# Kernel optimization log

Measured on AMD Instinct MI355X. Metric: run time of the kernel, lower is better.

Reference implementation:

```python
import jax, jax.numpy as jnp
import numpy as np

S_CENTROIDS = 512
RADIUS = 0.5
NSAMPLE = 32
BN_EPS = 1e-5


def farthest_point_sample(xyz, s):
    # xyz: [B, N, 3] -> idx [B, s], deterministic start at index 0
    B, N, _ = xyz.shape

    def step(carry, _):
        dist, far = carry  # dist [B,N], far [B]
        centroid = jnp.take_along_axis(xyz, far[:, None, None], axis=1)  # [B,1,3]
        d = jnp.sum((xyz - centroid) ** 2, axis=-1)  # [B,N]
        dist = jnp.minimum(dist, d)
        nxt = jnp.argmax(dist, axis=-1).astype(jnp.int32)
        return (dist, nxt), far

    init = (jnp.full((B, N), 1e10, dtype=xyz.dtype), jnp.zeros((B,), jnp.int32))
    _, idx = jax.lax.scan(step, init, None, length=s)
    return idx.T  # [B, s]


def query_ball_point(radius, nsample, xyz, new_xyz):
    # xyz [B,N,3], new_xyz [B,S,3] -> group idx [B,S,nsample]
    B, N, _ = xyz.shape
    sqr = jnp.sum((new_xyz[:, :, None, :] - xyz[:, None, :, :]) ** 2, axis=-1)  # [B,S,N]
    gidx = jnp.where(sqr > radius * radius, N, jnp.arange(N, dtype=jnp.int32)[None, None, :])
    gidx = jnp.sort(gidx, axis=-1)[:, :, :nsample]  # closest-index-first valid ids
    first = gidx[:, :, :1]
    gidx = jnp.where(gidx == N, first, gidx)  # pad misses with first neighbor
    return gidx


def bn_relu(h, gamma, beta):
    # training-mode BatchNorm1d over (batch, length) dims of [BS, C, k]
    m = jnp.mean(h, axis=(0, 2), keepdims=True)
    v = jnp.var(h, axis=(0, 2), keepdims=True)
    hn = (h - m) / jnp.sqrt(v + BN_EPS)
    return jax.nn.relu(hn * gamma[None, :, None] + beta[None, :, None])


def setup_inputs() -> dict:
    key = jax.random.key(0)
    k1, k2, k3, k4 = jax.random.split(key, 4)
    B, N, Din, Dout = 16, 2048, 64, 128  # in_channels=2*Din=128
    x = jax.random.normal(k1, (B, Din, N), dtype=jnp.float32)
    coords = jax.random.uniform(k2, (B, N, 3), dtype=jnp.float32, minval=-1.0, maxval=1.0)
    W1 = jax.random.normal(k3, (Dout, 2 * Din), dtype=jnp.float32) * 0.05  # conv1 1x1 kernel
    W2 = jax.random.normal(k4, (Dout, Dout), dtype=jnp.float32) * 0.05    # conv2 1x1 kernel
    gamma1 = jnp.ones((Dout,), jnp.float32); beta1 = jnp.zeros((Dout,), jnp.float32)
    gamma2 = jnp.ones((Dout,), jnp.float32); beta2 = jnp.zeros((Dout,), jnp.float32)
    return {"x": x, "coords": coords, "W1": W1, "W2": W2,
            "gamma1": gamma1, "beta1": beta1, "gamma2": gamma2, "beta2": beta2}


def reference(x, coords, W1, W2, gamma1, beta1, gamma2, beta2):
    B = x.shape[0]
    feats = jnp.transpose(x, (0, 2, 1))  # [B, N, D]

    fidx = farthest_point_sample(coords, S_CENTROIDS)  # [B, s]
    bidx = jnp.arange(B)[:, None]
    new_xyz = coords[bidx, fidx]        # [B, s, 3]
    new_feat = feats[bidx, fidx]        # [B, s, D]

    gidx = query_ball_point(RADIUS, NSAMPLE, coords, new_xyz)  # [B, s, k]
    grouped = feats[jnp.arange(B)[:, None, None], gidx]        # [B, s, k, D]

    center = new_feat[:, :, None, :]
    agg = jnp.concatenate([grouped - center,
                           jnp.broadcast_to(center, grouped.shape)], axis=-1)  # [B, s, k, 2D]

    b, s, k, d = agg.shape
    h = jnp.transpose(agg, (0, 1, 3, 2)).reshape(b * s, d, k)  # [BS, 2D, k]
    h = bn_relu(jnp.einsum('bck,oc->bok', h, W1), gamma1, beta1)
    h = bn_relu(jnp.einsum('bck,oc->bok', h, W2), gamma2, beta2)
    pooled = jnp.max(h, axis=-1)                  # [BS, out]
    new_feature = jnp.transpose(pooled.reshape(b, s, -1), (0, 2, 1))  # [B, out, s]
    return new_xyz, new_feature
```

## Files before the change

kernel.cpp:

```cpp
#include <hip/hip_runtime.h>
#include <cstdint>

typedef unsigned int uint;
typedef unsigned short ushort_t;
typedef unsigned long long ull;
typedef __attribute__((ext_vector_type(8))) short bf16x8;
typedef __attribute__((ext_vector_type(4))) float f32x4;
typedef __attribute__((ext_vector_type(2))) float f32x2;

#define B_   16
#define N_   2048
#define S_   512
#define G_   8192
#define DIN  64
#define DOUT 128
#define K_   32
#define ATS  136
#define ATS1 72

__device__ __forceinline__ uint bf16b(float f) {
  uint u = __float_as_uint(f);
  return (u + 0x7fffu + ((u >> 16) & 1u)) >> 16;
}
__device__ __forceinline__ float bf2f(uint b) { return __uint_as_float(b << 16); }

template<int CTRL, int RM>
__device__ __forceinline__ float dpp_fmax_step(float x) {
  float y = __uint_as_float((uint)__builtin_amdgcn_update_dpp(
      (int)__float_as_uint(x), (int)__float_as_uint(x), CTRL, RM, 0xf, true));
  return fmaxf(x, y);
}

__global__ __launch_bounds__(256) void fps_kernel(const float* __restrict__ coords,
                                                  int* __restrict__ fidx,
                                                  float* __restrict__ out_xyz) {
  int b = blockIdx.x;
  const float* cb = coords + (size_t)b * (N_ * 3);
  __shared__ float sptx[N_], spty[N_], sptz[N_];
  __shared__ ull   skey[2][4];
  __shared__ int   sfar[S_];
  int tid = threadIdx.x, lane = tid & 63, wid = tid >> 6;
  for (int j = tid; j < N_; j += 256) {
    sptx[j] = cb[3 * j]; spty[j] = cb[3 * j + 1]; sptz[j] = cb[3 * j + 2];
  }
  f32x2 px[4], py[4], pz[4], dist[4];
  int j0 = tid * 8;
#pragma unroll
  for (int p = 0; p < 4; ++p) {
    int j = j0 + 2 * p;
    px[p].x = cb[3 * j];     py[p].x = cb[3 * j + 1]; pz[p].x = cb[3 * j + 2];
    px[p].y = cb[3 * j + 3]; py[p].y = cb[3 * j + 4]; pz[p].y = cb[3 * j + 5];
    dist[p].x = 1e10f; dist[p].y = 1e10f;
  }
  float cx = cb[0], cy = cb[1], cz = cb[2];
  uint far = 0;
  __syncthreads();
  for (int s = 0; s < S_; ++s) {
    if (tid == 0) sfar[s] = (int)far;
    f32x2 c2x = {cx, cx}, c2y = {cy, cy}, c2z = {cz, cz};
    float bestv = -1.f; uint bestloc = 0;
#pragma unroll
    for (int p = 0; p < 4; ++p) {
      f32x2 dx, dy, dz, qx, qy, qz, s1, s2;
      asm("v_pk_add_f32 %0, %1, %2 neg_lo:[0,1] neg_hi:[0,1]" : "=v"(dx) : "v"(px[p]), "v"(c2x));
      asm("v_pk_add_f32 %0, %1, %2 neg_lo:[0,1] neg_hi:[0,1]" : "=v"(dy) : "v"(py[p]), "v"(c2y));
      asm("v_pk_add_f32 %0, %1, %2 neg_lo:[0,1] neg_hi:[0,1]" : "=v"(dz) : "v"(pz[p]), "v"(c2z));
      asm("v_pk_mul_f32 %0, %1, %1" : "=v"(qx) : "v"(dx));
      asm("v_pk_mul_f32 %0, %1, %1" : "=v"(qy) : "v"(dy));
      asm("v_pk_mul_f32 %0, %1, %1" : "=v"(qz) : "v"(dz));
      asm("v_pk_add_f32 %0, %1, %2" : "=v"(s1) : "v"(qx), "v"(qy));
      asm("v_pk_add_f32 %0, %1, %2" : "=v"(s2) : "v"(s1), "v"(qz));
      float n0 = fminf(dist[p].x, s2.x);
      float n1 = fminf(dist[p].y, s2.y);
      dist[p].x = n0; dist[p].y = n1;
      bool g0 = n0 > bestv; bestv = g0 ? n0 : bestv; bestloc = g0 ? (uint)(2 * p) : bestloc;
      bool g1 = n1 > bestv; bestv = g1 ? n1 : bestv; bestloc = g1 ? (uint)(2 * p + 1) : bestloc;
    }
    float m = bestv;
    m = dpp_fmax_step<0x111, 0xf>(m);
    m = dpp_fmax_step<0x112, 0xf>(m);
    m = dpp_fmax_step<0x114, 0xf>(m);
    m = dpp_fmax_step<0x118, 0xf>(m);
    m = dpp_fmax_step<0x142, 0xa>(m);
    m = dpp_fmax_step<0x143, 0xc>(m);
    float wmax = __uint_as_float((uint)__builtin_amdgcn_readlane((int)__float_as_uint(m), 63));
    ull mask = __ballot(bestv == wmax);
    int wl = __ffsll((long long)mask) - 1;
    uint loc = (uint)__builtin_amdgcn_readlane((int)bestloc, wl);
    uint jg = (uint)(((wid << 6) + wl) * 8) + loc;
    int pb = s & 1;
    if (lane == 0) skey[pb][wid] = ((ull)__float_as_uint(wmax) << 32) | (ull)(~jg);
    __syncthreads();
    ull k0 = skey[pb][0], k1 = skey[pb][1], k2 = skey[pb][2], k3 = skey[pb][3];
    uint w0 = ~(uint)k0, w1 = ~(uint)k1, w2 = ~(uint)k2, w3 = ~(uint)k3;
    float x0 = sptx[w0], y0 = spty[w0], z0 = sptz[w0];
    float x1 = sptx[w1], y1 = spty[w1], z1 = sptz[w1];
    float x2 = sptx[w2], y2 = spty[w2], z2 = sptz[w2];
    float x3 = sptx[w3], y3 = spty[w3], z3 = sptz[w3];
    bool t01 = k0 > k1, t23 = k2 > k3;
    ull ka = t01 ? k0 : k1;  float xa = t01 ? x0 : x1, ya = t01 ? y0 : y1, za = t01 ? z0 : z1;
    ull kb = t23 ? k2 : k3;  float xb = t23 ? x2 : x3, yb = t23 ? y2 : y3, zb = t23 ? z2 : z3;
    bool tw = ka > kb;
    far = ~(uint)(tw ? ka : kb);
    cx = tw ? xa : xb; cy = tw ? ya : yb; cz = tw ? za : zb;
  }
  __syncthreads();
  for (int s2 = tid; s2 < S_; s2 += 256) {
    int f = sfar[s2];
    fidx[b * S_ + s2] = f;
    int o = (b * S_ + s2) * 3;
    out_xyz[o] = sptx[f]; out_xyz[o + 1] = spty[f]; out_xyz[o + 2] = sptz[f];
  }
}

__global__ __launch_bounds__(256) void ball_kernel(const float* __restrict__ coords,
                                                   const int* __restrict__ fidx,
                                                   int* __restrict__ gidx) {
  int lane = threadIdx.x & 63;
  int g = __builtin_amdgcn_readfirstlane(blockIdx.x * 4 + (threadIdx.x >> 6));
  int b = g >> 9;
  const float* cb = coords + (size_t)b * (N_ * 3);
  int nf = fidx[g];
  float cx = cb[3 * nf], cy = cb[3 * nf + 1], cz = cb[3 * nf + 2];
  int* out = gidx + g * K_;
  int cnt = 0, first = 0;
  bool hasfirst = false;
  for (int base = 0; base < N_; base += 64) {
    int j = base + lane;
    float dx = __fsub_rn(cb[3 * j], cx);
    float dy = __fsub_rn(cb[3 * j + 1], cy);
    float dz = __fsub_rn(cb[3 * j + 2], cz);
    float d = __fadd_rn(__fadd_rn(__fmul_rn(dx, dx), __fmul_rn(dy, dy)), __fmul_rn(dz, dz));
    bool in = (d <= 0.25f);
    ull m = __ballot(in);
    if (in) {
      int pos = cnt + __popcll(m & ((1ull << lane) - 1ull));
      if (pos < K_) out[pos] = j;
    }
    if (!hasfirst && m) { first = base + (__ffsll((long long)m) - 1); hasfirst = true; }
    cnt += __popcll(m);
    if (cnt >= K_) break;
  }
  if (cnt < K_) {
    for (int p = cnt + lane; p < K_; p += 64) out[p] = first;
  }
}

__global__ __launch_bounds__(256) void prep_kernel(const float* __restrict__ W1,
                                                   const float* __restrict__ W2,
                                                   ushort_t* __restrict__ Bp1,
                                                   ushort_t* __restrict__ Bpd,
                                                   ushort_t* __restrict__ Bp2) {
  int i = blockIdx.x * 256 + threadIdx.x;
  int j2 = i & 7, l = (i >> 3) & 63;
  {
    int kc = (i >> 9) & 3, nt = i >> 11;
    int o2 = nt * 16 + (l & 15);
    int c2 = kc * 32 + ((l >> 4) * 8) + j2;
    Bp2[i] = (ushort_t)bf16b(W2[o2 * 128 + c2]);
  }
  if (i < 8192) {
    int kc = (i >> 9) & 1, nt = (i >> 10) & 7;
    int o2 = nt * 16 + (l & 15);
    int c2 = kc * 32 + ((l >> 4) * 8) + j2;
    float wa = W1[o2 * 128 + c2];
    float wb = W1[o2 * 128 + 64 + c2];
    Bp1[i] = (ushort_t)bf16b(wa);
    Bpd[i] = (ushort_t)bf16b(wb - wa);
  }
}

__global__ __launch_bounds__(256) void gemm1_kernel(const float* __restrict__ x,
    const int* __restrict__ fidx, const int* __restrict__ gidx,
    const ushort_t* __restrict__ Bp1, const ushort_t* __restrict__ Bpd,
    ushort_t* __restrict__ h1T, float* __restrict__ psum, float* __restrict__ psq) {
  __shared__ ushort_t xgT[4][32 * ATS1];
  __shared__ float sctr[4][DIN];
  int tid = threadIdx.x;
  int lane = tid & 63, wid = tid >> 6;
  int g = __builtin_amdgcn_readfirstlane(blockIdx.x * 4 + wid);
  int b = g >> 9;
  const float* xb = x + (size_t)b * (DIN * N_);
  int nf = fidx[g];
  sctr[wid][lane] = xb[(size_t)lane * N_ + nf];
  int kk = lane & 31, ch = lane >> 5;
  int gik = gidx[g * K_ + kk];
  ushort_t* xw = xgT[wid];
#pragma unroll
  for (int cc = 0; cc < 32; ++cc) {
    int c = ch * 32 + cc;
    xw[kk * ATS1 + c] = (ushort_t)bf16b(xb[(size_t)c * N_ + gik]);
  }
  __syncthreads();
  int l15 = lane & 15, r8 = (lane >> 4) * 8;
  f32x4 acc[2][8];
#pragma unroll
  for (int nt = 0; nt < 8; ++nt) acc[0][nt] = (f32x4){0.f, 0.f, 0.f, 0.f};
#pragma unroll
  for (int kc = 0; kc < 2; ++kc) {
    union { bf16x8 v; ushort_t u[8]; } cu;
#pragma unroll
    for (int j = 0; j < 8; ++j) cu.u[j] = (ushort_t)bf16b(sctr[wid][kc * 32 + r8 + j]);
#pragma unroll
    for (int nt = 0; nt < 8; ++nt) {
      bf16x8 bf = *(const bf16x8*)(Bpd + ((nt * 2 + kc) * 64 + lane) * 8);
      acc[0][nt] = __builtin_amdgcn_mfma_f32_16x16x32_bf16(cu.v, bf, acc[0][nt], 0, 0, 0);
    }
  }
#pragma unroll
  for (int nt = 0; nt < 8; ++nt) acc[1][nt] = acc[0][nt];
#pragma unroll
  for (int kc = 0; kc < 2; ++kc) {
    bf16x8 afrag[2];
#pragma unroll
    for (int mt = 0; mt < 2; ++mt)
      afrag[mt] = *(const bf16x8*)(xw + (mt * 16 + l15) * ATS1 + kc * 32 + r8);
#pragma unroll
    for (int nt = 0; nt < 8; ++nt) {
      bf16x8 bf = *(const bf16x8*)(Bp1 + ((nt * 2 + kc) * 64 + lane) * 8);
      acc[0][nt] = __builtin_amdgcn_mfma_f32_16x16x32_bf16(afrag[0], bf, acc[0][nt], 0, 0, 0);
      acc[1][nt] = __builtin_amdgcn_mfma_f32_16x16x32_bf16(afrag[1], bf, acc[1][nt], 0, 0, 0);
    }
  }
#pragma unroll
  for (int nt = 0; nt < 8; ++nt) {
    float s = 0.f, q = 0.f;
#pragma unroll
    for (int mt = 0; mt < 2; ++mt)
#pragma unroll
      for (int r = 0; r < 4; ++r) { float a = acc[mt][nt][r]; s += a; q = fmaf(a, a, q); }
    s += __shfl_xor(s, 16, 64); s += __shfl_xor(s, 32, 64);
    q += __shfl_xor(q, 16, 64); q += __shfl_xor(q, 32, 64);
    if (lane < 16) {
      int o = nt * 16 + lane;
      psum[o * G_ + g] = s; psq[o * G_ + g] = q;
    }
  }
#pragma unroll
  for (int mt = 0; mt < 2; ++mt)
#pragma unroll
    for (int r = 0; r < 4; ++r) {
      int k = mt * 16 + (lane >> 4) * 4 + r;
      ushort_t* dst = h1T + (size_t)g * 4096 + k * 128 + l15;
#pragma unroll
      for (int nt = 0; nt < 8; ++nt)
        dst[nt * 16] = (ushort_t)bf16b(acc[mt][nt][r]);
    }
}

__global__ __launch_bounds__(256) void bn_finalize(const float* __restrict__ psum,
    const float* __restrict__ psq, const float* __restrict__ gamma,
    const float* __restrict__ beta, float* __restrict__ bnp) {
  int o = blockIdx.x, tid = threadIdx.x;
  double s = 0.0, q = 0.0;
  for (int g = tid; g < G_; g += 256) { s += (double)psum[o * G_ + g]; q += (double)psq[o * G_ + g]; }
  __shared__ double ss[256], qq[256];
  ss[tid] = s; qq[tid] = q; __syncthreads();
  for (int off = 128; off > 0; off >>= 1) {
    if (tid < off) { ss[tid] += ss[tid + off]; qq[tid] += qq[tid + off]; }
    __syncthreads();
  }
  if (tid == 0) {
    double n = 262144.0;
    double mean = ss[0] / n, var = qq[0] / n - mean * mean;
    float scv = (float)((double)gamma[o] / sqrt(var + 1e-5));
    bnp[2 * o] = scv;
    bnp[2 * o + 1] = (float)((double)beta[o] - mean * (double)scv);
  }
}

__global__ __launch_bounds__(256) void gemm2_kernel(const ushort_t* __restrict__ h1T,
    const ushort_t* __restrict__ Bp2, const float* __restrict__ bnp1,
    float* __restrict__ psum, float* __restrict__ psq,
    float* __restrict__ hmax, float* __restrict__ hmin) {
  __shared__ ushort_t actT[4][32 * ATS];
  int tid = threadIdx.x;
  int lane = tid & 63, wid = tid >> 6;
  int g = __builtin_amdgcn_readfirstlane(blockIdx.x * 4 + wid);
  ushort_t* aw = actT[wid];
  int c0 = (lane & 15) * 8;
  float s1[8], t1[8];
#pragma unroll
  for (int jj = 0; jj < 8; ++jj) { s1[jj] = bnp1[2 * (c0 + jj)]; t1[jj] = bnp1[2 * (c0 + jj) + 1]; }
  const uint4* src = (const uint4*)(h1T + (size_t)g * 4096);
#pragma unroll
  for (int t = 0; t < 8; ++t) {
    int idx = t * 64 + lane;
    uint4 v = src[idx];
    int k = idx >> 4;
    uint w[4] = {v.x, v.y, v.z, v.w};
    uint o4[4];
#pragma unroll
    for (int p2 = 0; p2 < 4; ++p2) {
      float a0 = fmaxf(fmaf(bf2f(w[p2] & 0xffffu), s1[2 * p2], t1[2 * p2]), 0.f);
      float a1 = fmaxf(fmaf(bf2f(w[p2] >> 16), s1[2 * p2 + 1], t1[2 * p2 + 1]), 0.f);
      o4[p2] = (bf16b(a1) << 16) | bf16b(a0);
    }
    *(uint4*)(aw + k * ATS + c0) = make_uint4(o4[0], o4[1], o4[2], o4[3]);
  }
  __syncthreads();
  f32x4 acc[2][8];
#pragma unroll
  for (int mt = 0; mt < 2; ++mt)
#pragma unroll
    for (int nt = 0; nt < 8; ++nt) acc[mt][nt] = (f32x4){0.f, 0.f, 0.f, 0.f};
#pragma unroll
  for (int kc = 0; kc < 4; ++kc) {
    bf16x8 afrag[2];
#pragma unroll
    for (int mt = 0; mt < 2; ++mt)
      afrag[mt] = *(const bf16x8*)(aw + (mt * 16 + (lane & 15)) * ATS + kc * 32 + (lane >> 4) * 8);
#pragma unroll
    for (int nt = 0; nt < 8; ++nt) {
      bf16x8 bfrag = *(const bf16x8*)(Bp2 + ((nt * 4 + kc) * 64 + lane) * 8);
      acc[0][nt] = __builtin_amdgcn_mfma_f32_16x16x32_bf16(afrag[0], bfrag, acc[0][nt], 0, 0, 0);
      acc[1][nt] = __builtin_amdgcn_mfma_f32_16x16x32_bf16(afrag[1], bfrag, acc[1][nt], 0, 0, 0);
    }
  }
#pragma unroll
  for (int nt = 0; nt < 8; ++nt) {
    float s = 0.f, q = 0.f, mx = -1e30f, mn = 1e30f;
#pragma unroll
    for (int mt = 0; mt < 2; ++mt)
#pragma unroll
      for (int r = 0; r < 4; ++r) {
        float a = acc[mt][nt][r];
        s += a; q = fmaf(a, a, q); mx = fmaxf(mx, a); mn = fminf(mn, a);
      }
    s += __shfl_xor(s, 16, 64); s += __shfl_xor(s, 32, 64);
    q += __shfl_xor(q, 16, 64); q += __shfl_xor(q, 32, 64);
    mx = fmaxf(mx, __shfl_xor(mx, 16, 64)); mx = fmaxf(mx, __shfl_xor(mx, 32, 64));
    mn = fminf(mn, __shfl_xor(mn, 16, 64)); mn = fminf(mn, __shfl_xor(mn, 32, 64));
    if (lane < 16) {
      int o = nt * 16 + lane;
      psum[o * G_ + g] = s; psq[o * G_ + g] = q;
      hmax[o * G_ + g] = mx; hmin[o * G_ + g] = mn;
    }
  }
}

__global__ __launch_bounds__(256) void pool_kernel(const float* __restrict__ hmax,
    const float* __restrict__ hmin, const float* __restrict__ bnp2,
    float* __restrict__ out) {
  int i = blockIdx.x * 256 + threadIdx.x;
  int s = i & 511;
  int o = (i >> 9) & 127;
  int b = i >> 16;
  int g = b * 512 + s;
  float scv = bnp2[2 * o], tf = bnp2[2 * o + 1];
  float v = (scv >= 0.f) ? hmax[o * G_ + g] : hmin[o * G_ + g];
  out[i] = fmaxf(fmaf(scv, v, tf), 0.f);
}

extern "C" void kernel_launch(void* const* d_in, const int* in_sizes, int n_in,
                              void* d_out, int out_size, void* d_ws, size_t ws_size,
                              hipStream_t stream) {
  const float* x      = (const float*)d_in[0];
  const float* coords = (const float*)d_in[1];
  const float* W1     = (const float*)d_in[2];
  const float* W2     = (const float*)d_in[3];
  const float* gamma1 = (const float*)d_in[4];
  const float* beta1  = (const float*)d_in[5];
  const float* gamma2 = (const float*)d_in[6];
  const float* beta2  = (const float*)d_in[7];
  float* out = (float*)d_out;
  char* ws = (char*)d_ws;
  ushort_t* h1T  = (ushort_t*)(ws);
  float* psum1 = (float*)(ws + 67108864);
  float* psq1  = (float*)(ws + 71303168);
  float* psum2 = (float*)(ws + 75497472);
  float* psq2  = (float*)(ws + 79691776);
  float* hmax  = (float*)(ws + 83886080);
  float* hmin  = (float*)(ws + 88080384);
  ushort_t* Bp1 = (ushort_t*)(ws + 92274688);
  ushort_t* Bpd = (ushort_t*)(ws + 92291072);
  ushort_t* Bp2 = (ushort_t*)(ws + 92307456);
  float* bnp1  = (float*)(ws + 92340224);
  float* bnp2  = (float*)(ws + 92341248);
  int* fidx    = (int*)(ws + 92342272);
  int* gidx    = (int*)(ws + 92375040);

  prep_kernel<<<64, 256, 0, stream>>>(W1, W2, Bp1, Bpd, Bp2);
  fps_kernel<<<16, 256, 0, stream>>>(coords, fidx, out);
  ball_kernel<<<2048, 256, 0, stream>>>(coords, fidx, gidx);
  gemm1_kernel<<<2048, 256, 0, stream>>>(x, fidx, gidx, Bp1, Bpd, h1T, psum1, psq1);
  bn_finalize<<<128, 256, 0, stream>>>(psum1, psq1, gamma1, beta1, bnp1);
  gemm2_kernel<<<2048, 256, 0, stream>>>(h1T, Bp2, bnp1, psum2, psq2, hmax, hmin);
  bn_finalize<<<128, 256, 0, stream>>>(psum2, psq2, gamma2, beta2, bnp2);
  pool_kernel<<<4096, 256, 0, stream>>>(hmax, hmin, bnp2, out + 24576);
}
```

Baseline: 382.8 us.

## Fuse ball query into gemm1 and carry FPS candidate coords via readlane

The ball-query kernel is removed and its per-wave neighbor search now runs at the start of gemm1, writing group indices to shared memory instead of a global buffer. This saves one kernel launch and a global write/read round trip. In FPS, each wave now picks its candidate's coordinates from registers by readlane and publishes them through shared memory next to the key. That replaces four dependent LDS gathers on the serial per-iteration critical path. The cost is more VGPR selects per iteration and extra work in gemm1 before its gather.

```diff
diff --git a/kernel.cpp b/kernel.cpp
--- a/kernel.cpp
+++ b/kernel.cpp
@@ -37,8 +37,9 @@
   int b = blockIdx.x;
   const float* cb = coords + (size_t)b * (N_ * 3);
   __shared__ float sptx[N_], spty[N_], sptz[N_];
-  __shared__ ull   skey[2][4];
-  __shared__ int   sfar[S_];
+  __shared__ ull    skey[2][4];
+  __shared__ float4 scand[2][4];
+  __shared__ int    sfar[S_];
   int tid = threadIdx.x, lane = tid & 63, wid = tid >> 6;
   for (int j = tid; j < N_; j += 256) {
     sptx[j] = cb[3 * j]; spty[j] = cb[3 * j + 1]; sptz[j] = cb[3 * j + 2];
@@ -76,6 +77,16 @@
       bool g0 = n0 > bestv; bestv = g0 ? n0 : bestv; bestloc = g0 ? (uint)(2 * p) : bestloc;
       bool g1 = n1 > bestv; bestv = g1 ? n1 : bestv; bestloc = g1 ? (uint)(2 * p + 1) : bestloc;
     }
+    bool h = (bestloc & 1u) != 0, qb0 = (bestloc & 2u) != 0, qb1 = (bestloc & 4u) != 0;
+    float ax0 = h ? px[0].y : px[0].x, ax1 = h ? px[1].y : px[1].x;
+    float ax2 = h ? px[2].y : px[2].x, ax3 = h ? px[3].y : px[3].x;
+    float bx = qb1 ? (qb0 ? ax3 : ax2) : (qb0 ? ax1 : ax0);
+    float ay0 = h ? py[0].y : py[0].x, ay1 = h ? py[1].y : py[1].x;
+    float ay2 = h ? py[2].y : py[2].x, ay3 = h ? py[3].y : py[3].x;
+    float by = qb1 ? (qb0 ? ay3 : ay2) : (qb0 ? ay1 : ay0);
+    float az0 = h ? pz[0].y : pz[0].x, az1 = h ? pz[1].y : pz[1].x;
+    float az2 = h ? pz[2].y : pz[2].x, az3 = h ? pz[3].y : pz[3].x;
+    float bz = qb1 ? (qb0 ? az3 : az2) : (qb0 ? az1 : az0);
     float m = bestv;
     m = dpp_fmax_step<0x111, 0xf>(m);
     m = dpp_fmax_step<0x112, 0xf>(m);
@@ -87,22 +98,25 @@
     ull mask = __ballot(bestv == wmax);
     int wl = __ffsll((long long)mask) - 1;
     uint loc = (uint)__builtin_amdgcn_readlane((int)bestloc, wl);
+    float wx = __uint_as_float((uint)__builtin_amdgcn_readlane((int)__float_as_uint(bx), wl));
+    float wy = __uint_as_float((uint)__builtin_amdgcn_readlane((int)__float_as_uint(by), wl));
+    float wz = __uint_as_float((uint)__builtin_amdgcn_readlane((int)__float_as_uint(bz), wl));
     uint jg = (uint)(((wid << 6) + wl) * 8) + loc;
     int pb = s & 1;
-    if (lane == 0) skey[pb][wid] = ((ull)__float_as_uint(wmax) << 32) | (ull)(~jg);
+    if (lane == 0) {
+      skey[pb][wid] = ((ull)__float_as_uint(wmax) << 32) | (ull)(~jg);
+      scand[pb][wid] = make_float4(wx, wy, wz, 0.f);
+    }
     __syncthreads();
     ull k0 = skey[pb][0], k1 = skey[pb][1], k2 = skey[pb][2], k3 = skey[pb][3];
-    uint w0 = ~(uint)k0, w1 = ~(uint)k1, w2 = ~(uint)k2, w3 = ~(uint)k3;
-    float x0 = sptx[w0], y0 = spty[w0], z0 = sptz[w0];
-    float x1 = sptx[w1], y1 = spty[w1], z1 = sptz[w1];
-    float x2 = sptx[w2], y2 = spty[w2], z2 = sptz[w2];
-    float x3 = sptx[w3], y3 = spty[w3], z3 = sptz[w3];
+    float4 q0 = scand[pb][0], q1 = scand[pb][1], q2 = scand[pb][2], q3 = scand[pb][3];
     bool t01 = k0 > k1, t23 = k2 > k3;
-    ull ka = t01 ? k0 : k1;  float xa = t01 ? x0 : x1, ya = t01 ? y0 : y1, za = t01 ? z0 : z1;
-    ull kb = t23 ? k2 : k3;  float xb = t23 ? x2 : x3, yb = t23 ? y2 : y3, zb = t23 ? z2 : z3;
-    bool tw = ka > kb;
-    far = ~(uint)(tw ? ka : kb);
-    cx = tw ? xa : xb; cy = tw ? ya : yb; cz = tw ? za : zb;
+    ull ka = t01 ? k0 : k1;   float4 qa = t01 ? q0 : q1;
+    ull kb2 = t23 ? k2 : k3;  float4 qb4 = t23 ? q2 : q3;
+    bool tw = ka > kb2;
+    far = ~(uint)(tw ? ka : kb2);
+    float4 qw = tw ? qa : qb4;
+    cx = qw.x; cy = qw.y; cz = qw.z;
   }
   __syncthreads();
   for (int s2 = tid; s2 < S_; s2 += 256) {
@@ -110,39 +124,6 @@
     fidx[b * S_ + s2] = f;
     int o = (b * S_ + s2) * 3;
     out_xyz[o] = sptx[f]; out_xyz[o + 1] = spty[f]; out_xyz[o + 2] = sptz[f];
-  }
-}
-
-__global__ __launch_bounds__(256) void ball_kernel(const float* __restrict__ coords,
-                                                   const int* __restrict__ fidx,
-                                                   int* __restrict__ gidx) {
-  int lane = threadIdx.x & 63;
-  int g = __builtin_amdgcn_readfirstlane(blockIdx.x * 4 + (threadIdx.x >> 6));
-  int b = g >> 9;
-  const float* cb = coords + (size_t)b * (N_ * 3);
-  int nf = fidx[g];
-  float cx = cb[3 * nf], cy = cb[3 * nf + 1], cz = cb[3 * nf + 2];
-  int* out = gidx + g * K_;
-  int cnt = 0, first = 0;
-  bool hasfirst = false;
-  for (int base = 0; base < N_; base += 64) {
-    int j = base + lane;
-    float dx = __fsub_rn(cb[3 * j], cx);
-    float dy = __fsub_rn(cb[3 * j + 1], cy);
-    float dz = __fsub_rn(cb[3 * j + 2], cz);
-    float d = __fadd_rn(__fadd_rn(__fmul_rn(dx, dx), __fmul_rn(dy, dy)), __fmul_rn(dz, dz));
-    bool in = (d <= 0.25f);
-    ull m = __ballot(in);
-    if (in) {
-      int pos = cnt + __popcll(m & ((1ull << lane) - 1ull));
-      if (pos < K_) out[pos] = j;
-    }
-    if (!hasfirst && m) { first = base + (__ffsll((long long)m) - 1); hasfirst = true; }
-    cnt += __popcll(m);
-    if (cnt >= K_) break;
-  }
-  if (cnt < K_) {
-    for (int p = cnt + lane; p < K_; p += 64) out[p] = first;
   }
 }
 
@@ -171,20 +152,46 @@
 }
 
 __global__ __launch_bounds__(256) void gemm1_kernel(const float* __restrict__ x,
-    const int* __restrict__ fidx, const int* __restrict__ gidx,
+    const float* __restrict__ coords, const int* __restrict__ fidx,
     const ushort_t* __restrict__ Bp1, const ushort_t* __restrict__ Bpd,
     ushort_t* __restrict__ h1T, float* __restrict__ psum, float* __restrict__ psq) {
   __shared__ ushort_t xgT[4][32 * ATS1];
   __shared__ float sctr[4][DIN];
+  __shared__ int sgidx[4][K_];
   int tid = threadIdx.x;
   int lane = tid & 63, wid = tid >> 6;
   int g = __builtin_amdgcn_readfirstlane(blockIdx.x * 4 + wid);
   int b = g >> 9;
   const float* xb = x + (size_t)b * (DIN * N_);
+  const float* cb = coords + (size_t)b * (N_ * 3);
   int nf = fidx[g];
+  {
+    float cx = cb[3 * nf], cy = cb[3 * nf + 1], cz = cb[3 * nf + 2];
+    int cnt = 0, first = 0;
+    bool hasfirst = false;
+    for (int base = 0; base < N_; base += 64) {
+      int j = base + lane;
+      float dx = __fsub_rn(cb[3 * j], cx);
+      float dy = __fsub_rn(cb[3 * j + 1], cy);
+      float dz = __fsub_rn(cb[3 * j + 2], cz);
+      float d = __fadd_rn(__fadd_rn(__fmul_rn(dx, dx), __fmul_rn(dy, dy)), __fmul_rn(dz, dz));
+      bool in = (d <= 0.25f);
+      ull m = __ballot(in);
+      if (in) {
+        int pos = cnt + __popcll(m & ((1ull << lane) - 1ull));
+        if (pos < K_) sgidx[wid][pos] = j;
+      }
+      if (!hasfirst && m) { first = base + (__ffsll((long long)m) - 1); hasfirst = true; }
+      cnt += __popcll(m);
+      if (cnt >= K_) break;
+    }
+    if (cnt < K_) {
+      for (int p = cnt + lane; p < K_; p += 64) sgidx[wid][p] = first;
+    }
+  }
   sctr[wid][lane] = xb[(size_t)lane * N_ + nf];
   int kk = lane & 31, ch = lane >> 5;
-  int gik = gidx[g * K_ + kk];
+  int gik = sgidx[wid][kk];
   ushort_t* xw = xgT[wid];
 #pragma unroll
   for (int cc = 0; cc < 32; ++cc) {
@@ -378,12 +385,10 @@
   float* bnp1  = (float*)(ws + 92340224);
   float* bnp2  = (float*)(ws + 92341248);
   int* fidx    = (int*)(ws + 92342272);
-  int* gidx    = (int*)(ws + 92375040);
 
   prep_kernel<<<64, 256, 0, stream>>>(W1, W2, Bp1, Bpd, Bp2);
   fps_kernel<<<16, 256, 0, stream>>>(coords, fidx, out);
-  ball_kernel<<<2048, 256, 0, stream>>>(coords, fidx, gidx);
-  gemm1_kernel<<<2048, 256, 0, stream>>>(x, fidx, gidx, Bp1, Bpd, h1T, psum1, psq1);
+  gemm1_kernel<<<2048, 256, 0, stream>>>(x, coords, fidx, Bp1, Bpd, h1T, psum1, psq1);
   bn_finalize<<<128, 256, 0, stream>>>(psum1, psq1, gamma1, beta1, bnp1);
   gemm2_kernel<<<2048, 256, 0, stream>>>(h1T, Bp2, bnp1, psum2, psq2, hmax, hmin);
   bn_finalize<<<128, 256, 0, stream>>>(psum2, psq2, gamma2, beta2, bnp2);
```

Measured after the change: 463.1 us. 21.0% more time.

## Pre-transpose features to bf16 point-major and fuse ball query into gemm1

Applied to the files above, without the earlier changes.

A new transpose kernel writes x as bf16 in [B, N, 64] point-major layout into a reused workspace region. gemm1 then loads its MFMA A-fragments directly from global memory with contiguous 16-byte gathers, replacing the old strided per-channel gathers and the LDS staging tile. The ball-query search is moved into gemm1, with each wave keeping its neighbour list in shared memory, so the separate ball kernel launch and its gidx round trip are gone. The cost is an extra full pass over x, and the xT buffer aliases the psum2/psq2 workspace, which is only safe because those are written after gemm1.

```diff
diff --git a/kernel.cpp b/kernel.cpp
--- a/kernel.cpp
+++ b/kernel.cpp
@@ -16,7 +16,6 @@
 #define DOUT 128
 #define K_   32
 #define ATS  136
-#define ATS1 72
 
 __device__ __forceinline__ uint bf16b(float f) {
   uint u = __float_as_uint(f);
@@ -113,36 +112,23 @@
   }
 }
 
-__global__ __launch_bounds__(256) void ball_kernel(const float* __restrict__ coords,
-                                                   const int* __restrict__ fidx,
-                                                   int* __restrict__ gidx) {
-  int lane = threadIdx.x & 63;
-  int g = __builtin_amdgcn_readfirstlane(blockIdx.x * 4 + (threadIdx.x >> 6));
-  int b = g >> 9;
-  const float* cb = coords + (size_t)b * (N_ * 3);
-  int nf = fidx[g];
-  float cx = cb[3 * nf], cy = cb[3 * nf + 1], cz = cb[3 * nf + 2];
-  int* out = gidx + g * K_;
-  int cnt = 0, first = 0;
-  bool hasfirst = false;
-  for (int base = 0; base < N_; base += 64) {
-    int j = base + lane;
-    float dx = __fsub_rn(cb[3 * j], cx);
-    float dy = __fsub_rn(cb[3 * j + 1], cy);
-    float dz = __fsub_rn(cb[3 * j + 2], cz);
-    float d = __fadd_rn(__fadd_rn(__fmul_rn(dx, dx), __fmul_rn(dy, dy)), __fmul_rn(dz, dz));
-    bool in = (d <= 0.25f);
-    ull m = __ballot(in);
-    if (in) {
-      int pos = cnt + __popcll(m & ((1ull << lane) - 1ull));
-      if (pos < K_) out[pos] = j;
-    }
-    if (!hasfirst && m) { first = base + (__ffsll((long long)m) - 1); hasfirst = true; }
-    cnt += __popcll(m);
-    if (cnt >= K_) break;
-  }
-  if (cnt < K_) {
-    for (int p = cnt + lane; p < K_; p += 64) out[p] = first;
+__global__ __launch_bounds__(256) void txp_kernel(const float* __restrict__ x,
+                                                  ushort_t* __restrict__ xT) {
+  __shared__ float tile[64][65];
+  int b = blockIdx.x >> 5;
+  int n0 = (blockIdx.x & 31) * 64;
+  int nn = threadIdx.x & 63, c4 = threadIdx.x >> 6;
+  const float* xb = x + (size_t)b * (DIN * N_);
+#pragma unroll
+  for (int i = 0; i < 16; ++i) {
+    int c = c4 * 16 + i;
+    tile[nn][c] = xb[(size_t)c * N_ + n0 + nn];
+  }
+  __syncthreads();
+#pragma unroll
+  for (int i = 0; i < 16; ++i) {
+    int n = c4 * 16 + i;
+    xT[((size_t)b * N_ + n0 + n) * 64 + nn] = (ushort_t)bf16b(tile[n][nn]);
   }
 }
 
@@ -170,56 +156,68 @@
   }
 }
 
-__global__ __launch_bounds__(256) void gemm1_kernel(const float* __restrict__ x,
-    const int* __restrict__ fidx, const int* __restrict__ gidx,
+__global__ __launch_bounds__(256) void gemm1_kernel(const ushort_t* __restrict__ xT,
+    const float* __restrict__ coords, const int* __restrict__ fidx,
     const ushort_t* __restrict__ Bp1, const ushort_t* __restrict__ Bpd,
     ushort_t* __restrict__ h1T, float* __restrict__ psum, float* __restrict__ psq) {
-  __shared__ ushort_t xgT[4][32 * ATS1];
-  __shared__ float sctr[4][DIN];
+  __shared__ int sgidx[4][K_];
   int tid = threadIdx.x;
   int lane = tid & 63, wid = tid >> 6;
   int g = __builtin_amdgcn_readfirstlane(blockIdx.x * 4 + wid);
   int b = g >> 9;
-  const float* xb = x + (size_t)b * (DIN * N_);
+  const float* cb = coords + (size_t)b * (N_ * 3);
   int nf = fidx[g];
-  sctr[wid][lane] = xb[(size_t)lane * N_ + nf];
-  int kk = lane & 31, ch = lane >> 5;
-  int gik = gidx[g * K_ + kk];
-  ushort_t* xw = xgT[wid];
-#pragma unroll
-  for (int cc = 0; cc < 32; ++cc) {
-    int c = ch * 32 + cc;
-    xw[kk * ATS1 + c] = (ushort_t)bf16b(xb[(size_t)c * N_ + gik]);
-  }
-  __syncthreads();
+  {
+    float cx = cb[3 * nf], cy = cb[3 * nf + 1], cz = cb[3 * nf + 2];
+    int cnt = 0, first = 0;
+    bool hasfirst = false;
+    for (int base = 0; base < N_; base += 64) {
+      int j = base + lane;
+      float dx = __fsub_rn(cb[3 * j], cx);
+      float dy = __fsub_rn(cb[3 * j + 1], cy);
+      float dz = __fsub_rn(cb[3 * j + 2], cz);
+      float d = __fadd_rn(__fadd_rn(__fmul_rn(dx, dx), __fmul_rn(dy, dy)), __fmul_rn(dz, dz));
+      bool in = (d <= 0.25f);
+      ull m = __ballot(in);
+      if (in) {
+        int pos = cnt + __popcll(m & ((1ull << lane) - 1ull));
+        if (pos < K_) sgidx[wid][pos] = j;
+      }
+      if (!hasfirst && m) { first = base + (__ffsll((long long)m) - 1); hasfirst = true; }
+      cnt += __popcll(m);
+      if (cnt >= K_) break;
+    }
+    if (cnt < K_) {
+      for (int p = cnt + lane; p < K_; p += 64) sgidx[wid][p] = first;
+    }
+  }
   int l15 = lane & 15, r8 = (lane >> 4) * 8;
+  const ushort_t* xb64 = xT + (size_t)b * N_ * 64;
   f32x4 acc[2][8];
 #pragma unroll
   for (int nt = 0; nt < 8; ++nt) acc[0][nt] = (f32x4){0.f, 0.f, 0.f, 0.f};
 #pragma unroll
   for (int kc = 0; kc < 2; ++kc) {
-    union { bf16x8 v; ushort_t u[8]; } cu;
-#pragma unroll
-    for (int j = 0; j < 8; ++j) cu.u[j] = (ushort_t)bf16b(sctr[wid][kc * 32 + r8 + j]);
+    bf16x8 cu = *(const bf16x8*)(xb64 + nf * 64 + kc * 32 + r8);
 #pragma unroll
     for (int nt = 0; nt < 8; ++nt) {
       bf16x8 bf = *(const bf16x8*)(Bpd + ((nt * 2 + kc) * 64 + lane) * 8);
-      acc[0][nt] = __builtin_amdgcn_mfma_f32_16x16x32_bf16(cu.v, bf, acc[0][nt], 0, 0, 0);
+      acc[0][nt] = __builtin_amdgcn_mfma_f32_16x16x32_bf16(cu, bf, acc[0][nt], 0, 0, 0);
     }
   }
 #pragma unroll
   for (int nt = 0; nt < 8; ++nt) acc[1][nt] = acc[0][nt];
+  int gi0 = sgidx[wid][l15];
+  int gi1 = sgidx[wid][16 + l15];
 #pragma unroll
   for (int kc = 0; kc < 2; ++kc) {
-    bf16x8 afrag[2];
-#pragma unroll
-    for (int mt = 0; mt < 2; ++mt)
-      afrag[mt] = *(const bf16x8*)(xw + (mt * 16 + l15) * ATS1 + kc * 32 + r8);
+    bf16x8 af0 = *(const bf16x8*)(xb64 + (size_t)gi0 * 64 + kc * 32 + r8);
+    bf16x8 af1 = *(const bf16x8*)(xb64 + (size_t)gi1 * 64 + kc * 32 + r8);
 #pragma unroll
     for (int nt = 0; nt < 8; ++nt) {
       bf16x8 bf = *(const bf16x8*)(Bp1 + ((nt * 2 + kc) * 64 + lane) * 8);
-      acc[0][nt] = __builtin_amdgcn_mfma_f32_16x16x32_bf16(afrag[0], bf, acc[0][nt], 0, 0, 0);
-      acc[1][nt] = __builtin_amdgcn_mfma_f32_16x16x32_bf16(afrag[1], bf, acc[1][nt], 0, 0, 0);
+      acc[0][nt] = __builtin_amdgcn_mfma_f32_16x16x32_bf16(af0, bf, acc[0][nt], 0, 0, 0);
+      acc[1][nt] = __builtin_amdgcn_mfma_f32_16x16x32_bf16(af1, bf, acc[1][nt], 0, 0, 0);
     }
   }
 #pragma unroll
@@ -370,6 +368,7 @@
   float* psq1  = (float*)(ws + 71303168);
   float* psum2 = (float*)(ws + 75497472);
   float* psq2  = (float*)(ws + 79691776);
+  ushort_t* xT = (ushort_t*)(ws + 75497472);
   float* hmax  = (float*)(ws + 83886080);
   float* hmin  = (float*)(ws + 88080384);
   ushort_t* Bp1 = (ushort_t*)(ws + 92274688);
@@ -378,12 +377,11 @@
   float* bnp1  = (float*)(ws + 92340224);
   float* bnp2  = (float*)(ws + 92341248);
   int* fidx    = (int*)(ws + 92342272);
-  int* gidx    = (int*)(ws + 92375040);
-
+
+  txp_kernel<<<512, 256, 0, stream>>>(x, xT);
   prep_kernel<<<64, 256, 0, stream>>>(W1, W2, Bp1, Bpd, Bp2);
   fps_kernel<<<16, 256, 0, stream>>>(coords, fidx, out);
-  ball_kernel<<<2048, 256, 0, stream>>>(coords, fidx, gidx);
-  gemm1_kernel<<<2048, 256, 0, stream>>>(x, fidx, gidx, Bp1, Bpd, h1T, psum1, psq1);
+  gemm1_kernel<<<2048, 256, 0, stream>>>(xT, coords, fidx, Bp1, Bpd, h1T, psum1, psq1);
   bn_finalize<<<128, 256, 0, stream>>>(psum1, psq1, gamma1, beta1, bnp1);
   gemm2_kernel<<<2048, 256, 0, stream>>>(h1T, Bp2, bnp1, psum2, psq2, hmax, hmin);
   bn_finalize<<<128, 256, 0, stream>>>(psum2, psq2, gamma2, beta2, bnp2);
```

New measurement: 354.9 us. -7.3%, faster.
